# Kernel tuning notes

Measured on AMD Instinct MI355X. Metric: run time of the kernel, lower is better.

Reference implementation:

```python
import jax, jax.numpy as jnp
import numpy as np

BLOCK_SIZE = 256
N_EMBD = 768
HEAD_SIZE = 768  # == n_embd so RoPE table (dim=n_embd) matches channel pairing


def _rope_tables(T, dim, theta0=10000.0):
    # compute_freq(dim=n_embd, seq_len=block_size, theta_0=10000):
    # theta_j = theta0^(-2j/dim), angle[t, j] = t * theta_j
    j = jnp.arange(dim // 2, dtype=jnp.float32)
    theta = jnp.float32(theta0) ** (-2.0 * j / jnp.float32(dim))
    ang = jnp.arange(T, dtype=jnp.float32)[:, None] * theta[None, :]  # [T, dim/2]
    return jnp.cos(ang), jnp.sin(ang)


def _apply_rope(t, cos, sin):
    # t: [B, T, D]; pair adjacent channels (2j, 2j+1) as complex, rotate.
    B, T, D = t.shape
    tr = t.reshape(B, T, D // 2, 2)
    re, im = tr[..., 0], tr[..., 1]
    out_re = re * cos[None] - im * sin[None]
    out_im = re * sin[None] + im * cos[None]
    return jnp.stack([out_re, out_im], axis=-1).reshape(B, T, D)


def setup_inputs() -> dict:
    key = jax.random.key(0)
    k1, k2, k3, k4 = jax.random.split(key, 4)
    B, T = 128, BLOCK_SIZE
    x = jax.random.normal(k1, (B, T, N_EMBD), dtype=jnp.float32)
    Wq = jax.random.normal(k2, (N_EMBD, HEAD_SIZE), dtype=jnp.float32) * 0.02
    Wk = jax.random.normal(k3, (N_EMBD, HEAD_SIZE), dtype=jnp.float32) * 0.02
    Wv = jax.random.normal(k4, (N_EMBD, HEAD_SIZE), dtype=jnp.float32) * 0.02
    return {"x": x, "Wq": Wq, "Wk": Wk, "Wv": Wv}


def reference(x, Wq, Wk, Wv):
    B, T, C = x.shape
    q = x @ Wq  # [B, T, D]
    k = x @ Wk
    v = x @ Wv
    cos, sin = _rope_tables(T, HEAD_SIZE)
    q = _apply_rope(q, cos, sin)
    k = _apply_rope(k, cos, sin)
    scale = jnp.float32(HEAD_SIZE) ** -0.5
    wei = jnp.einsum('bqd,bkd->bqk', q, k) * scale  # [B, T, T]
    causal = jnp.tril(jnp.ones((T, T), dtype=bool))
    wei = jnp.where(causal[None], wei, -jnp.inf)
    wei = jax.nn.softmax(wei, axis=-1)
    # dropout(p=0.2) is identity in eval/deterministic baseline
    out = jnp.einsum('bqk,bkd->bqd', wei, v)  # [B, T, D]
    return out
```

## Files before the change

### kernel.cpp

```cpp
#include <hip/hip_runtime.h>
#include <hip/hip_bf16.h>
#include <stdint.h>


typedef __attribute__((ext_vector_type(8))) short short8;
typedef __attribute__((ext_vector_type(4))) short short4v;
typedef __attribute__((ext_vector_type(4))) float f32x4;

__device__ __forceinline__ short f2bf(float f) {
    uint32_t u = __float_as_uint(f);
    u += 0x7fffu + ((u >> 16) & 1u);
    return (short)(u >> 16);
}

__global__ __launch_bounds__(256) void cvt_x(const float* __restrict__ x,
                                             short* __restrict__ xb) {
    long i = ((long)blockIdx.x * 256 + threadIdx.x) * 4;
    f32x4 v = *(const f32x4*)(x + i);
    short4v o;
    o.x = f2bf(v.x); o.y = f2bf(v.y); o.z = f2bf(v.z); o.w = f2bf(v.w);
    *(short4v*)(xb + i) = o;
}

__global__ __launch_bounds__(256) void cvt_wt(const float* __restrict__ W,
                                              short* __restrict__ Wt) {
    __shared__ float tile[32][33];
    int d0 = blockIdx.x * 32, c0 = blockIdx.y * 32;
    int tr = threadIdx.x >> 5, tc = threadIdx.x & 31;
    #pragma unroll
    for (int i = 0; i < 32; i += 8)
        tile[tr + i][tc] = W[(long)(c0 + tr + i) * 768 + d0 + tc];
    __syncthreads();
    #pragma unroll
    for (int i = 0; i < 32; i += 8)
        Wt[(long)(d0 + tr + i) * 768 + c0 + tc] = f2bf(tile[tc][tr + i]);
}

__global__ __launch_bounds__(256) void rope_tab(float2* __restrict__ rt) {
    int i = blockIdx.x * 256 + threadIdx.x;
    int t = i / 384, j = i - t * 384;
    const float CE = -0.034603417655f;
    float th = exp2f((float)j * CE);
    float s, c;
    sincosf((float)t * th, &s, &c);
    rt[i] = make_float2(c, s);
}

__global__ __launch_bounds__(512, 2)
void qkv256(const short* __restrict__ A, const short* __restrict__ B,
            short* __restrict__ Q, short* __restrict__ Kb,
            short* __restrict__ Vt, const float2* __restrict__ rt) {
    int p = blockIdx.x;
    int c = p & 7, j = p >> 3;
    int st = j / 9;
    int bx = j - st * 9;
    int by = c * 16 + st;
    const int m0 = by * 256, n0 = bx * 256;

    __shared__ short lA[2][256 * 64];
    __shared__ short lB[2][256 * 64];

    const int tid = threadIdx.x;
    const int w = tid >> 6, lane = tid & 63;
    const int wm = (w >> 2) * 128;
    const int wn = (w & 3) * 64;
    const int lr8 = lane >> 3;
    const int scol = (((lane & 7) - lr8) & 7) * 8;
    const int fr = lane & 15, kq = lane >> 4;

    f32x4 acc[8][4] = {};
    short8 af[4][2];
    short8 bq[4][2];

#define STAGE_HALF(lX, gX, r0g, h, t) do {                                     \
    int _buf = (t) & 1;                                                        \
    _Pragma("unroll")                                                          \
    for (int _i = 0; _i < 2; ++_i) {                                           \
        int _rl = (h) * 128 + (w * 2 + _i) * 8;                                \
        const short* _g = (gX) + (long)((r0g) + _rl + lr8) * 768               \
                               + (t) * 64 + scol;                              \
        __builtin_amdgcn_global_load_lds(                                      \
            (const __attribute__((address_space(1))) void*)_g,                 \
            (__attribute__((address_space(3))) void*)(&lX[_buf][_rl * 64]),    \
            16, 0, 0);                                                         \
    }                                                                          \
} while (0)

#define LOAD_A(mh, buf) do {                                                   \
    _Pragma("unroll")                                                          \
    for (int _t = 0; _t < 4; ++_t)                                             \
        _Pragma("unroll")                                                      \
        for (int _k = 0; _k < 2; ++_k)                                         \
            af[_t][_k] = *(const short8*)(&lA[buf][                            \
                (wm + (mh) * 64 + _t * 16 + fr) * 64 +                         \
                ((_k * 4 + kq + fr) & 7) * 8]);                                \
} while (0)

#define LOAD_B(nh, buf) do {                                                   \
    _Pragma("unroll")                                                          \
    for (int _t = 0; _t < 2; ++_t)                                             \
        _Pragma("unroll")                                                      \
        for (int _k = 0; _k < 2; ++_k)                                         \
            bq[(nh) * 2 + _t][_k] = *(const short8*)(&lB[buf][                 \
                (wn + (nh) * 32 + _t * 16 + fr) * 64 +                         \
                ((_k * 4 + kq + fr) & 7) * 8]);                                \
} while (0)

#define MMA_Q(mh, nh) do {                                                     \
    __builtin_amdgcn_s_setprio(1);                                             \
    _Pragma("unroll")                                                          \
    for (int _t = 0; _t < 4; ++_t)                                             \
        _Pragma("unroll")                                                      \
        for (int _n = 0; _n < 2; ++_n)                                         \
            _Pragma("unroll")                                                  \
            for (int _k = 0; _k < 2; ++_k)                                     \
                acc[(mh) * 4 + _t][(nh) * 2 + _n] =                            \
                    __builtin_amdgcn_mfma_f32_16x16x32_bf16(                   \
                        af[_t][_k], bq[(nh) * 2 + _n][_k],                     \
                        acc[(mh) * 4 + _t][(nh) * 2 + _n], 0, 0, 0);           \
    __builtin_amdgcn_s_setprio(0);                                             \
} while (0)

#define BAR() __builtin_amdgcn_s_barrier()
#define LGKM0() asm volatile("s_waitcnt lgkmcnt(0)" ::: "memory")
#define VMC4() asm volatile("s_waitcnt vmcnt(4)" ::: "memory")
#define VMC0() asm volatile("s_waitcnt vmcnt(0)" ::: "memory")

    STAGE_HALF(lB, B, n0, 0, 0);
    STAGE_HALF(lB, B, n0, 1, 0);
    STAGE_HALF(lA, A, m0, 0, 0);
    STAGE_HALF(lA, A, m0, 1, 0);
    STAGE_HALF(lB, B, n0, 0, 1);
    STAGE_HALF(lB, B, n0, 1, 1);
    VMC4();
    BAR();

    #pragma unroll 1
    for (int i = 0; i < 6; ++i) {
        const int t0 = 2 * i;
        const bool more = (i < 5);
        LOAD_A(0, 0); LOAD_B(0, 0);
        STAGE_HALF(lA, A, m0, 0, t0 + 1);
        BAR(); LGKM0(); MMA_Q(0, 0); BAR();
        LOAD_B(1, 0);
        STAGE_HALF(lA, A, m0, 1, t0 + 1);
        BAR(); LGKM0(); MMA_Q(0, 1); BAR();
        LOAD_A(1, 0);
        if (more) STAGE_HALF(lB, B, n0, 0, t0 + 2);
        BAR(); LGKM0(); MMA_Q(1, 1); BAR();
        if (more) STAGE_HALF(lB, B, n0, 1, t0 + 2);
        BAR(); LGKM0(); MMA_Q(1, 0);
        if (more) { VMC4(); } else { VMC0(); }
        BAR();
        LOAD_A(0, 1); LOAD_B(0, 1);
        if (more) STAGE_HALF(lA, A, m0, 0, t0 + 2);
        BAR(); LGKM0(); MMA_Q(0, 0); BAR();
        LOAD_B(1, 1);
        if (more) STAGE_HALF(lA, A, m0, 1, t0 + 2);
        BAR(); LGKM0(); MMA_Q(0, 1); BAR();
        LOAD_A(1, 1);
        if (more) STAGE_HALF(lB, B, n0, 0, t0 + 3);
        BAR(); LGKM0(); MMA_Q(1, 1); BAR();
        if (more) STAGE_HALF(lB, B, n0, 1, t0 + 3);
        BAR(); LGKM0(); MMA_Q(1, 0);
        if (more) VMC4();
        BAR();
    }

    const int type = (bx >= 6) ? 2 : (bx >= 3 ? 1 : 0);
    const int nl0 = n0 - type * 768;
    const int r0 = wm + (lane >> 4) * 4;
    const int c0 = wn + (lane & 15);
    if (type < 2) {
        short* dst = (type == 0) ? Q : Kb;
        const int par = lane & 1;
        #pragma unroll
        for (int tmi = 0; tmi < 8; ++tmi)
            #pragma unroll
            for (int tni = 0; tni < 4; ++tni) {
                int col = nl0 + c0 + tni * 16;
                const float2* rtc = rt + (col >> 1);
                #pragma unroll
                for (int r = 0; r < 4; ++r) {
                    int row = m0 + r0 + tmi * 16 + r;
                    float val = acc[tmi][tni][r];
                    float pv = __shfl_xor(val, 1);
                    float2 cs = rtc[(row & 255) * 384];
                    float re = par ? pv : val;
                    float im = par ? val : pv;
                    float o = par ? (re * cs.y + im * cs.x)
                                  : (re * cs.x - im * cs.y);
                    dst[(long)row * 768 + col] = f2bf(o);
                }
            }
    } else {
        #pragma unroll
        for (int tmi = 0; tmi < 8; ++tmi)
            #pragma unroll
            for (int tni = 0; tni < 4; ++tni) {
                int col = nl0 + c0 + tni * 16;
                #pragma unroll
                for (int r = 0; r < 4; ++r) {
                    int row = m0 + r0 + tmi * 16 + r;
                    Vt[((long)(row >> 8) * 768 + col) * 256 + (row & 255)] =
                        f2bf(acc[tmi][tni][r]);
                }
            }
    }
#undef STAGE_HALF
#undef LOAD_A
#undef LOAD_B
#undef MMA_Q
#undef BAR
#undef LGKM0
#undef VMC4
#undef VMC0
}

__global__ __launch_bounds__(512)
void s_softmax(const short* __restrict__ Qm, const short* __restrict__ Km,
               short* __restrict__ P, float scale) {
    int p = blockIdx.x;
    int c = p & 7, j = p >> 3;
    int bz = c * 16 + (j >> 1);
    int mh = j & 1;
    const short* Ab = Qm + (long)bz * 196608 + (long)mh * 98304;
    const short* Bb = Km + (long)bz * 196608;

    __shared__ short lA[128 * 64];
    __shared__ short lB[256 * 64];

    const int tid = threadIdx.x;
    const int w = tid >> 6, lane = tid & 63;
    const int wm = (w >> 2) * 64;
    const int wn = (w & 3) * 64;
    const int lr8 = lane >> 3;
    const int scol = (((lane & 7) - lr8) & 7) * 8;
    const int fr = lane & 15, kq = lane >> 4;

    f32x4 acc[4][4] = {};

    for (int k0 = 0; k0 < 768; k0 += 64) {
        #pragma unroll
        for (int i = 0; i < 2; ++i) {
            int seg = i * 8 + w;
            const short* ga = Ab + (long)(seg * 8 + lr8) * 768 + k0 + scol;
            __builtin_amdgcn_global_load_lds(
                (const __attribute__((address_space(1))) void*)ga,
                (__attribute__((address_space(3))) void*)(lA + seg * 512),
                16, 0, 0);
        }
        #pragma unroll
        for (int i = 0; i < 4; ++i) {
            int seg = i * 8 + w;
            const short* gb = Bb + (long)(seg * 8 + lr8) * 768 + k0 + scol;
            __builtin_amdgcn_global_load_lds(
                (const __attribute__((address_space(1))) void*)gb,
                (__attribute__((address_space(3))) void*)(lB + seg * 512),
                16, 0, 0);
        }
        __syncthreads();
        #pragma unroll
        for (int cc = 0; cc < 2; ++cc) {
            const int sphys = ((cc * 4 + kq + fr) & 7) * 8;
            short8 afr[4], bfr[4];
            #pragma unroll
            for (int tmi = 0; tmi < 4; ++tmi)
                afr[tmi] = *(const short8*)(lA + (wm + fr + tmi * 16) * 64 + sphys);
            #pragma unroll
            for (int tni = 0; tni < 4; ++tni)
                bfr[tni] = *(const short8*)(lB + (wn + fr + tni * 16) * 64 + sphys);
            #pragma unroll
            for (int tmi = 0; tmi < 4; ++tmi)
                #pragma unroll
                for (int tni = 0; tni < 4; ++tni)
                    acc[tmi][tni] = __builtin_amdgcn_mfma_f32_16x16x32_bf16(
                        afr[tmi], bfr[tni], acc[tmi][tni], 0, 0, 0);
        }
        __syncthreads();
    }

    const int r0 = (lane >> 4) * 4;
    const int cb = lane & 15;
    const int nw = w & 3;
    float* redm = (float*)lA;
    float* reds = redm + 512;

    float M[16];
    #pragma unroll
    for (int tmi = 0; tmi < 4; ++tmi)
        #pragma unroll
        for (int r = 0; r < 4; ++r) {
            int rowL = wm + tmi * 16 + r0 + r;
            int tloc = mh * 128 + rowL;
            float m = -1e30f;
            #pragma unroll
            for (int tni = 0; tni < 4; ++tni) {
                int col = wn + cb + tni * 16;
                float v = (col <= tloc) ? acc[tmi][tni][r] * scale : -1e30f;
                acc[tmi][tni][r] = v;
                m = fmaxf(m, v);
            }
            m = fmaxf(m, __shfl_xor(m, 1));
            m = fmaxf(m, __shfl_xor(m, 2));
            m = fmaxf(m, __shfl_xor(m, 4));
            m = fmaxf(m, __shfl_xor(m, 8));
            M[tmi * 4 + r] = m;
        }
    if (cb == 0) {
        #pragma unroll
        for (int tmi = 0; tmi < 4; ++tmi)
            #pragma unroll
            for (int r = 0; r < 4; ++r)
                redm[(wm + tmi * 16 + r0 + r) * 4 + nw] = M[tmi * 4 + r];
    }
    __syncthreads();
    #pragma unroll
    for (int tmi = 0; tmi < 4; ++tmi)
        #pragma unroll
        for (int r = 0; r < 4; ++r) {
            f32x4 v = *(const f32x4*)(redm + (wm + tmi * 16 + r0 + r) * 4);
            M[tmi * 4 + r] = fmaxf(fmaxf(v.x, v.y), fmaxf(v.z, v.w));
        }
    float Sm[16];
    #pragma unroll
    for (int tmi = 0; tmi < 4; ++tmi)
        #pragma unroll
        for (int r = 0; r < 4; ++r) {
            float mm = M[tmi * 4 + r];
            float s = 0.f;
            #pragma unroll
            for (int tni = 0; tni < 4; ++tni) {
                float e = __expf(acc[tmi][tni][r] - mm);
                acc[tmi][tni][r] = e;
                s += e;
            }
            s += __shfl_xor(s, 1);
            s += __shfl_xor(s, 2);
            s += __shfl_xor(s, 4);
            s += __shfl_xor(s, 8);
            Sm[tmi * 4 + r] = s;
        }
    if (cb == 0) {
        #pragma unroll
        for (int tmi = 0; tmi < 4; ++tmi)
            #pragma unroll
            for (int r = 0; r < 4; ++r)
                reds[(wm + tmi * 16 + r0 + r) * 4 + nw] = Sm[tmi * 4 + r];
    }
    __syncthreads();
    const long rowBase = (long)bz * 256 + mh * 128;
    #pragma unroll
    for (int tmi = 0; tmi < 4; ++tmi)
        #pragma unroll
        for (int r = 0; r < 4; ++r) {
            int rowL = wm + tmi * 16 + r0 + r;
            f32x4 v = *(const f32x4*)(reds + rowL * 4);
            float inv = 1.0f / (v.x + v.y + v.z + v.w);
            short* pr = P + (rowBase + rowL) * 256;
            #pragma unroll
            for (int tni = 0; tni < 4; ++tni)
                pr[wn + cb + tni * 16] = f2bf(acc[tmi][tni][r] * inv);
        }
}

template <int EPI, int CAUSAL, int SWZ>
__global__ __launch_bounds__(256)
void gemm_bt(const short* __restrict__ A, const short* __restrict__ B,
             void* __restrict__ C, void* __restrict__ C2, void* __restrict__ C3,
             const float2* __restrict__ rt,
             int M, int N, int K, long sA, long sB, long sC, float scale) {
    int bx, by, bz;
    if (SWZ == 3) {
        int p = blockIdx.x + 6 * (blockIdx.y + 2 * blockIdx.z);
        int c = p & 7, j = p >> 3;
        int bt = j / 12;
        bz = c * 16 + bt;
        int t = j - bt * 12;
        by = t / 6; bx = t - (t / 6) * 6;
    } else {
        bx = blockIdx.x; by = blockIdx.y; bz = blockIdx.z;
    }
    const int m0 = by * 128;
    const int n0 = bx * 128;
    if (CAUSAL == 1 && n0 > m0) return;

    __shared__ short lA[128 * 64];
    __shared__ short lB[128 * 64];
    const short* Ab = A + (long)bz * sA;
    const short* Bb = B + (long)bz * sB;
    const int tid = threadIdx.x;
    const int w = tid >> 6, lane = tid & 63;
    const int wm = (w >> 1) * 64;
    const int wn = (w & 1) * 64;
    const int lrow8 = lane >> 3;
    const int lcol = (((lane & 7) - lrow8) & 7) * 8;
    const int fr = lane & 15;
    const int kq = lane >> 4;

    const int Kend = (CAUSAL == 2) ? (m0 + 128 < K ? m0 + 128 : K) : K;

    f32x4 acc[4][4] = {};

    for (int k0 = 0; k0 < Kend; k0 += 64) {
        #pragma unroll
        for (int i = 0; i < 4; ++i) {
            int seg = i * 4 + w;
            int row = seg * 8 + lrow8;
            const short* ga = Ab + (long)(m0 + row) * K + k0 + lcol;
            __builtin_amdgcn_global_load_lds(
                (const __attribute__((address_space(1))) void*)ga,
                (__attribute__((address_space(3))) void*)(lA + seg * 512),
                16, 0, 0);
            const short* gb = Bb + (long)(n0 + row) * K + k0 + lcol;
            __builtin_amdgcn_global_load_lds(
                (const __attribute__((address_space(1))) void*)gb,
                (__attribute__((address_space(3))) void*)(lB + seg * 512),
                16, 0, 0);
        }
        __syncthreads();

        #pragma unroll
        for (int c = 0; c < 2; ++c) {
            const int sphys = ((c * 4 + kq + fr) & 7) * 8;
            short8 afr[4], bfr[4];
            #pragma unroll
            for (int tmi = 0; tmi < 4; ++tmi)
                afr[tmi] = *(const short8*)(lA + (wm + fr + tmi * 16) * 64 + sphys);
            #pragma unroll
            for (int tni = 0; tni < 4; ++tni)
                bfr[tni] = *(const short8*)(lB + (wn + fr + tni * 16) * 64 + sphys);
            #pragma unroll
            for (int tmi = 0; tmi < 4; ++tmi)
                #pragma unroll
                for (int tni = 0; tni < 4; ++tni)
                    acc[tmi][tni] = __builtin_amdgcn_mfma_f32_16x16x32_bf16(
                        afr[tmi], bfr[tni], acc[tmi][tni], 0, 0, 0);
        }
        __syncthreads();
    }

    const int r0 = wm + (lane >> 4) * 4;
    const int c0 = wn + (lane & 15);

    if (EPI == 2) {
        #pragma unroll
        for (int tmi = 0; tmi < 4; ++tmi)
            #pragma unroll
            for (int tni = 0; tni < 4; ++tni)
                #pragma unroll
                for (int r = 0; r < 4; ++r) {
                    int row = m0 + r0 + tmi * 16 + r;
                    int col = n0 + c0 + tni * 16;
                    ((float*)C)[(long)bz * sC + (long)row * N + col] =
                        acc[tmi][tni][r] * scale;
                }
    }
}

extern "C" void kernel_launch(void* const* d_in, const int* in_sizes, int n_in,
                              void* d_out, int out_size, void* d_ws, size_t ws_size,
                              hipStream_t stream) {
    const float* x  = (const float*)d_in[0];
    const float* Wq = (const float*)d_in[1];
    const float* Wk = (const float*)d_in[2];
    const float* Wv = (const float*)d_in[3];

    char* ws = (char*)d_ws;
    short*  xb = (short*)(ws);
    short*  wt = (short*)(ws + 50331648);
    short*  qb = (short*)(ws + 53870592);
    short*  kb = (short*)(ws + 104202240);
    short*  vt = (short*)(ws + 154533888);
    short*  P  = (short*)(ws + 238419968);
    float2* rt = (float2*)(ws + 255197184);

    cvt_x<<<24576, 256, 0, stream>>>(x, xb);
    dim3 gw(24, 24);
    cvt_wt<<<gw, 256, 0, stream>>>(Wq, wt);
    cvt_wt<<<gw, 256, 0, stream>>>(Wk, wt + 589824);
    cvt_wt<<<gw, 256, 0, stream>>>(Wv, wt + 1179648);
    rope_tab<<<384, 256, 0, stream>>>(rt);

    qkv256<<<1152, 512, 0, stream>>>(xb, wt, qb, kb, vt, rt);

    s_softmax<<<256, 512, 0, stream>>>(qb, kb, P, 0.0360843918f);

    dim3 g3(6, 2, 128);
    gemm_bt<2, 2, 3><<<g3, 256, 0, stream>>>(P, vt, (float*)d_out, nullptr,
                                             nullptr, nullptr, 256, 768, 256,
                                             65536, 196608, 196608, 1.0f);
}
```

Before: 412.1 us.

## Fuse softmax and PV GEMM into one attention kernel with double-buffered staging

Merges the QK^T+softmax kernel and the P@V GEMM into a single kernel. The normalized probabilities stay in LDS as bf16 instead of round-tripping through global memory. The QK loop now double-buffers its Q/K tiles, and the PV phase streams V tiles with double buffering. This removes one launch and the P write/read traffic. In exchange it uses a much larger LDS footprint (about 132KB), which limits occupancy, and the causal skip now happens at block granularity per query half.

```diff
diff --git a/kernel.cpp b/kernel.cpp
--- a/kernel.cpp
+++ b/kernel.cpp
@@ -218,17 +218,18 @@
 }
 
 __global__ __launch_bounds__(512)
-void s_softmax(const short* __restrict__ Qm, const short* __restrict__ Km,
-               short* __restrict__ P, float scale) {
+void attn_fused(const short* __restrict__ Qm, const short* __restrict__ Km,
+                const short* __restrict__ Vm, float* __restrict__ out,
+                float scale) {
     int p = blockIdx.x;
     int c = p & 7, j = p >> 3;
     int bz = c * 16 + (j >> 1);
     int mh = j & 1;
     const short* Ab = Qm + (long)bz * 196608 + (long)mh * 98304;
     const short* Bb = Km + (long)bz * 196608;
-
-    __shared__ short lA[128 * 64];
-    __shared__ short lB[256 * 64];
+    const short* Vb = Vm + (long)bz * 196608;
+
+    __shared__ short smem[67584];
 
     const int tid = threadIdx.x;
     const int w = tid >> 6, lane = tid & 63;
@@ -237,39 +238,47 @@
     const int lr8 = lane >> 3;
     const int scol = (((lane & 7) - lr8) & 7) * 8;
     const int fr = lane & 15, kq = lane >> 4;
+    const int cb = fr;
 
     f32x4 acc[4][4] = {};
 
-    for (int k0 = 0; k0 < 768; k0 += 64) {
-        #pragma unroll
-        for (int i = 0; i < 2; ++i) {
-            int seg = i * 8 + w;
-            const short* ga = Ab + (long)(seg * 8 + lr8) * 768 + k0 + scol;
-            __builtin_amdgcn_global_load_lds(
-                (const __attribute__((address_space(1))) void*)ga,
-                (__attribute__((address_space(3))) void*)(lA + seg * 512),
-                16, 0, 0);
-        }
-        #pragma unroll
-        for (int i = 0; i < 4; ++i) {
-            int seg = i * 8 + w;
-            const short* gb = Bb + (long)(seg * 8 + lr8) * 768 + k0 + scol;
-            __builtin_amdgcn_global_load_lds(
-                (const __attribute__((address_space(1))) void*)gb,
-                (__attribute__((address_space(3))) void*)(lB + seg * 512),
-                16, 0, 0);
-        }
-        __syncthreads();
+#define GLL(g, l) __builtin_amdgcn_global_load_lds(                            \
+        (const __attribute__((address_space(1))) void*)(g),                    \
+        (__attribute__((address_space(3))) void*)(l), 16, 0, 0)
+
+#define STAGE_QK(t) do { int _b = (t) & 1;                                     \
+    _Pragma("unroll")                                                          \
+    for (int _i = 0; _i < 2; ++_i) { int _s = _i * 8 + w;                      \
+        GLL(Ab + (long)(_s * 8 + lr8) * 768 + (t) * 64 + scol,                 \
+            smem + _b * 8192 + _s * 512); }                                    \
+    _Pragma("unroll")                                                          \
+    for (int _i = 0; _i < 4; ++_i) { int _s = _i * 8 + w;                      \
+        GLL(Bb + (long)(_s * 8 + lr8) * 768 + (t) * 64 + scol,                 \
+            smem + 16384 + _b * 16384 + _s * 512); } } while (0)
+
+#define STAGE_V(dc, kc, b) do {                                                \
+    _Pragma("unroll")                                                          \
+    for (int _i = 0; _i < 2; ++_i) { int _s = _i * 8 + w;                      \
+        GLL(Vb + (long)((dc) * 128 + _s * 8 + lr8) * 256 + (kc) * 64 + scol,   \
+            smem + 49152 + (b) * 8192 + _s * 512); } } while (0)
+
+    STAGE_QK(0);
+    __syncthreads();
+    #pragma unroll 1
+    for (int t = 0; t < 12; ++t) {
+        if (t < 11) STAGE_QK(t + 1);
+        const short* la = smem + (t & 1) * 8192;
+        const short* lb = smem + 16384 + (t & 1) * 16384;
         #pragma unroll
         for (int cc = 0; cc < 2; ++cc) {
             const int sphys = ((cc * 4 + kq + fr) & 7) * 8;
             short8 afr[4], bfr[4];
             #pragma unroll
             for (int tmi = 0; tmi < 4; ++tmi)
-                afr[tmi] = *(const short8*)(lA + (wm + fr + tmi * 16) * 64 + sphys);
+                afr[tmi] = *(const short8*)(la + (wm + fr + tmi * 16) * 64 + sphys);
             #pragma unroll
             for (int tni = 0; tni < 4; ++tni)
-                bfr[tni] = *(const short8*)(lB + (wn + fr + tni * 16) * 64 + sphys);
+                bfr[tni] = *(const short8*)(lb + (wn + fr + tni * 16) * 64 + sphys);
             #pragma unroll
             for (int tmi = 0; tmi < 4; ++tmi)
                 #pragma unroll
@@ -280,10 +289,11 @@
         __syncthreads();
     }
 
-    const int r0 = (lane >> 4) * 4;
-    const int cb = lane & 15;
+    STAGE_V(0, 0, 0);
+
+    const int r0 = kq * 4;
     const int nw = w & 3;
-    float* redm = (float*)lA;
+    float* redm = (float*)(smem + 65536);
     float* reds = redm + 512;
 
     float M[16];
@@ -349,113 +359,72 @@
                 reds[(wm + tmi * 16 + r0 + r) * 4 + nw] = Sm[tmi * 4 + r];
     }
     __syncthreads();
-    const long rowBase = (long)bz * 256 + mh * 128;
+
+    short* Pch = smem + (w & 3) * 8192;
     #pragma unroll
     for (int tmi = 0; tmi < 4; ++tmi)
         #pragma unroll
         for (int r = 0; r < 4; ++r) {
             int rowL = wm + tmi * 16 + r0 + r;
-            f32x4 v = *(const f32x4*)(reds + rowL * 4);
-            float inv = 1.0f / (v.x + v.y + v.z + v.w);
-            short* pr = P + (rowBase + rowL) * 256;
-            #pragma unroll
-            for (int tni = 0; tni < 4; ++tni)
-                pr[wn + cb + tni * 16] = f2bf(acc[tmi][tni][r] * inv);
-        }
-}
-
-template <int EPI, int CAUSAL, int SWZ>
-__global__ __launch_bounds__(256)
-void gemm_bt(const short* __restrict__ A, const short* __restrict__ B,
-             void* __restrict__ C, void* __restrict__ C2, void* __restrict__ C3,
-             const float2* __restrict__ rt,
-             int M, int N, int K, long sA, long sB, long sC, float scale) {
-    int bx, by, bz;
-    if (SWZ == 3) {
-        int p = blockIdx.x + 6 * (blockIdx.y + 2 * blockIdx.z);
-        int c = p & 7, j = p >> 3;
-        int bt = j / 12;
-        bz = c * 16 + bt;
-        int t = j - bt * 12;
-        by = t / 6; bx = t - (t / 6) * 6;
-    } else {
-        bx = blockIdx.x; by = blockIdx.y; bz = blockIdx.z;
-    }
-    const int m0 = by * 128;
-    const int n0 = bx * 128;
-    if (CAUSAL == 1 && n0 > m0) return;
-
-    __shared__ short lA[128 * 64];
-    __shared__ short lB[128 * 64];
-    const short* Ab = A + (long)bz * sA;
-    const short* Bb = B + (long)bz * sB;
-    const int tid = threadIdx.x;
-    const int w = tid >> 6, lane = tid & 63;
-    const int wm = (w >> 1) * 64;
-    const int wn = (w & 1) * 64;
-    const int lrow8 = lane >> 3;
-    const int lcol = (((lane & 7) - lrow8) & 7) * 8;
-    const int fr = lane & 15;
-    const int kq = lane >> 4;
-
-    const int Kend = (CAUSAL == 2) ? (m0 + 128 < K ? m0 + 128 : K) : K;
-
-    f32x4 acc[4][4] = {};
-
-    for (int k0 = 0; k0 < Kend; k0 += 64) {
-        #pragma unroll
-        for (int i = 0; i < 4; ++i) {
-            int seg = i * 4 + w;
-            int row = seg * 8 + lrow8;
-            const short* ga = Ab + (long)(m0 + row) * K + k0 + lcol;
-            __builtin_amdgcn_global_load_lds(
-                (const __attribute__((address_space(1))) void*)ga,
-                (__attribute__((address_space(3))) void*)(lA + seg * 512),
-                16, 0, 0);
-            const short* gb = Bb + (long)(n0 + row) * K + k0 + lcol;
-            __builtin_amdgcn_global_load_lds(
-                (const __attribute__((address_space(1))) void*)gb,
-                (__attribute__((address_space(3))) void*)(lB + seg * 512),
-                16, 0, 0);
-        }
-        __syncthreads();
-
-        #pragma unroll
-        for (int c = 0; c < 2; ++c) {
-            const int sphys = ((c * 4 + kq + fr) & 7) * 8;
-            short8 afr[4], bfr[4];
-            #pragma unroll
-            for (int tmi = 0; tmi < 4; ++tmi)
-                afr[tmi] = *(const short8*)(lA + (wm + fr + tmi * 16) * 64 + sphys);
-            #pragma unroll
-            for (int tni = 0; tni < 4; ++tni)
-                bfr[tni] = *(const short8*)(lB + (wn + fr + tni * 16) * 64 + sphys);
-            #pragma unroll
-            for (int tmi = 0; tmi < 4; ++tmi)
-                #pragma unroll
-                for (int tni = 0; tni < 4; ++tni)
-                    acc[tmi][tni] = __builtin_amdgcn_mfma_f32_16x16x32_bf16(
-                        afr[tmi], bfr[tni], acc[tmi][tni], 0, 0, 0);
-        }
-        __syncthreads();
-    }
-
-    const int r0 = wm + (lane >> 4) * 4;
-    const int c0 = wn + (lane & 15);
-
-    if (EPI == 2) {
+            f32x4 sv = *(const f32x4*)(reds + rowL * 4);
+            float inv = 1.0f / (sv.x + sv.y + sv.z + sv.w);
+            #pragma unroll
+            for (int tni = 0; tni < 4; ++tni) {
+                int l = (cb >> 3) + tni * 2;
+                Pch[rowL * 64 + ((l + rowL) & 7) * 8 + (cb & 7)] =
+                    f2bf(acc[tmi][tni][r] * inv);
+            }
+        }
+    __syncthreads();
+
+    const int kcN = mh ? 4 : 2;
+    const int wn2 = (w & 3) * 32;
+    const long rowB = (long)bz * 256 + (long)mh * 128;
+    int vb = 0;
+    #pragma unroll 1
+    for (int dc = 0; dc < 6; ++dc) {
+        f32x4 a2[4][2] = {};
+        #pragma unroll 1
+        for (int kc = 0; kc < kcN; ++kc) {
+            int ndc = dc, nkc = kc + 1;
+            if (nkc == kcN) { ndc = dc + 1; nkc = 0; }
+            if (ndc < 6) STAGE_V(ndc, nkc, vb ^ 1);
+            const short* pch = smem + kc * 8192;
+            const short* lv = smem + 49152 + vb * 8192;
+            #pragma unroll
+            for (int cc = 0; cc < 2; ++cc) {
+                const int sp = ((cc * 4 + kq + fr) & 7) * 8;
+                short8 ap[4], bv[2];
+                #pragma unroll
+                for (int tmi = 0; tmi < 4; ++tmi)
+                    ap[tmi] = *(const short8*)(pch + (wm + tmi * 16 + fr) * 64 + sp);
+                #pragma unroll
+                for (int tn = 0; tn < 2; ++tn)
+                    bv[tn] = *(const short8*)(lv + (wn2 + tn * 16 + fr) * 64 + sp);
+                #pragma unroll
+                for (int tmi = 0; tmi < 4; ++tmi)
+                    #pragma unroll
+                    for (int tn = 0; tn < 2; ++tn)
+                        a2[tmi][tn] = __builtin_amdgcn_mfma_f32_16x16x32_bf16(
+                            ap[tmi], bv[tn], a2[tmi][tn], 0, 0, 0);
+            }
+            __syncthreads();
+            vb ^= 1;
+        }
         #pragma unroll
         for (int tmi = 0; tmi < 4; ++tmi)
             #pragma unroll
-            for (int tni = 0; tni < 4; ++tni)
+            for (int tn = 0; tn < 2; ++tn)
                 #pragma unroll
                 for (int r = 0; r < 4; ++r) {
-                    int row = m0 + r0 + tmi * 16 + r;
-                    int col = n0 + c0 + tni * 16;
-                    ((float*)C)[(long)bz * sC + (long)row * N + col] =
-                        acc[tmi][tni][r] * scale;
+                    long row = rowB + wm + tmi * 16 + kq * 4 + r;
+                    int col = dc * 128 + wn2 + tn * 16 + cb;
+                    out[row * 768 + col] = a2[tmi][tn][r];
                 }
     }
+#undef GLL
+#undef STAGE_QK
+#undef STAGE_V
 }
 
 extern "C" void kernel_launch(void* const* d_in, const int* in_sizes, int n_in,
@@ -472,7 +441,6 @@
     short*  qb = (short*)(ws + 53870592);
     short*  kb = (short*)(ws + 104202240);
     short*  vt = (short*)(ws + 154533888);
-    short*  P  = (short*)(ws + 238419968);
     float2* rt = (float2*)(ws + 255197184);
 
     cvt_x<<<24576, 256, 0, stream>>>(x, xb);
@@ -484,10 +452,6 @@
 
     qkv256<<<1152, 512, 0, stream>>>(xb, wt, qb, kb, vt, rt);
 
-    s_softmax<<<256, 512, 0, stream>>>(qb, kb, P, 0.0360843918f);
-
-    dim3 g3(6, 2, 128);
-    gemm_bt<2, 2, 3><<<g3, 256, 0, stream>>>(P, vt, (float*)d_out, nullptr,
-                                             nullptr, nullptr, 256, 768, 256,
-                                             65536, 196608, 196608, 1.0f);
-}
+    attn_fused<<<256, 512, 0, stream>>>(qb, kb, vt, (float*)d_out,
+                                        0.0360843918f);
+}
```

Measured after the change: 389.7 us. 5.4% less time.
